# Kernel optimization log

Hardware: AMD Instinct MI355X
Metric: run time of the kernel (lower is better)

Reference implementation:

```python
import jax, jax.numpy as jnp
import numpy as np
import math

C = 96; HEADS = 3; HD = C // HEADS; WS = 8; B = 4; H = 256; W = 256
EPS = 1e-5; SCALE = HD ** -0.5; LOGIT_MAX = math.log(1.0 / 0.01)
N = WS * WS


def _rel_pos():
    coords = np.stack(np.meshgrid(np.arange(WS), np.arange(WS), indexing='ij')).reshape(2, -1)
    rel = (coords[:, :, None] - coords[:, None, :]).transpose(1, 2, 0).astype(np.float32)
    return jnp.asarray(np.sign(rel) * np.log1p(np.abs(rel)))  # [N, N, 2]

REL = _rel_pos()


def conv1x1(x, w, b):
    return jnp.einsum('bchw,oc->bohw', x, w) + b[None, :, None, None]


def dwconv(x, w, b, pad, reflect=False):
    if reflect:
        x = jnp.pad(x, ((0, 0), (0, 0), (pad, pad), (pad, pad)), mode='reflect')
        padding = 'VALID'
    else:
        padding = [(pad, pad), (pad, pad)]
    y = jax.lax.conv_general_dilated(x, w, (1, 1), padding,
                                     feature_group_count=x.shape[1],
                                     dimension_numbers=('NCHW', 'OIHW', 'NCHW'))
    return y + b[None, :, None, None]


def window_partition(x):  # [B,H,W,C] -> [nW, WS*WS, C]
    b, h, w, c = x.shape
    x = x.reshape(b, h // WS, WS, w // WS, WS, c).transpose(0, 1, 3, 2, 4, 5)
    return x.reshape(-1, WS * WS, c)


def window_reverse(win, h, w):  # [nW, WS*WS, C] -> [B,H,W,C]
    b = win.shape[0] // ((h // WS) * (w // WS))
    x = win.reshape(b, h // WS, w // WS, WS, WS, -1).transpose(0, 1, 3, 2, 4, 5)
    return x.reshape(b, h, w, -1)


def setup_inputs() -> dict:
    key = jax.random.key(0)
    ks = jax.random.split(key, 16)
    def nrm(k, shape, std=0.02):
        return jax.random.normal(k, shape, jnp.float32) * std
    inp = {'x': jax.random.normal(ks[0], (B, C, H, W), jnp.float32)}
    inp.update(
        agn_weight=jnp.ones((C,), jnp.float32), agn_bias=jnp.zeros((C,), jnp.float32),
        meta1_w=nrm(ks[1], (C,)), meta1_b=jnp.ones((C,), jnp.float32),
        meta2_w=nrm(ks[2], (C,)), meta2_b=jnp.zeros((C,), jnp.float32),
        la1_w=nrm(ks[3], (C, 1, 3, 3)), la1_b=jnp.zeros((C,), jnp.float32),
        la2_w=nrm(ks[4], (C, 1, 3, 3)), la2_b=jnp.zeros((C,), jnp.float32),
        ta1_w=nrm(ks[5], (C, 1, 3, 3)), ta1_b=jnp.zeros((C,), jnp.float32),
        ta2_w=nrm(ks[6], (C, 1, 3, 3)), ta2_b=jnp.zeros((C,), jnp.float32),
        q_w=nrm(ks[7], (C, C)), q_b=jnp.zeros((C,), jnp.float32),
        kv_w=nrm(ks[8], (2 * C, C)), kv_b=jnp.zeros((2 * C,), jnp.float32),
        dw_w=nrm(ks[9], (C, 1, 5, 5)), dw_b=jnp.zeros((C,), jnp.float32),
        proj_w=nrm(ks[10], (C, C)), proj_b=jnp.zeros((C,), jnp.float32),
        logit_scale=jnp.asarray(math.log(1.0 / 0.07), jnp.float32),
        rp_w1=nrm(ks[11], (256, 2)), rp_b1=jnp.zeros((256,), jnp.float32),
        rp_w2=nrm(ks[12], (HEADS, 256)), rp_b2=jnp.zeros((HEADS,), jnp.float32),
        m1_w=nrm(ks[13], (4 * C, C)), m1_b=jnp.zeros((4 * C,), jnp.float32),
        m2_w=nrm(ks[14], (C, 4 * C)), m2_b=jnp.zeros((C,), jnp.float32),
    )
    return inp


def reference(x, agn_weight, agn_bias, meta1_w, meta1_b, meta2_w, meta2_b,
              la1_w, la1_b, la2_w, la2_b, ta1_w, ta1_b, ta2_w, ta2_b,
              q_w, q_b, kv_w, kv_b, dw_w, dw_b, proj_w, proj_b,
              logit_scale, rp_w1, rp_b1, rp_w2, rp_b2,
              m1_w, m1_b, m2_w, m2_b):
    identity = x
    # ---- AGN: per-sample global mean/std norm + dynamic affine + two dw-conv branches
    mean = jnp.mean(x, axis=(1, 2, 3), keepdims=True)                      # [B,1,1,1]
    std = jnp.sqrt(jnp.mean((x - mean) ** 2, axis=(1, 2, 3), keepdims=True) + EPS)
    xn = (x - mean) / std
    rescale = std * meta1_w[None, :, None, None] + meta1_b[None, :, None, None]   # conv1x1(1->C) on std
    rebias = mean * meta2_w[None, :, None, None] + meta2_b[None, :, None, None]
    local = dwconv(jax.nn.relu(dwconv(xn, la1_w, la1_b, 1)), la2_w, la2_b, 1)
    texture = dwconv(jax.nn.relu(dwconv(xn, ta1_w, ta1_b, 1)), ta2_w, ta2_b, 1)
    xn = xn * (agn_weight[None, :, None, None] * rescale) + (agn_bias[None, :, None, None] + rebias) + local + texture
    # ---- DSAttention (use_attn, DWConv, shift_size=0, H%WS==0 so no padding)
    Q = conv1x1(xn, q_w, q_b)
    KV = conv1x1(xn, kv_w, kv_b)                                           # [B,2C,H,W]
    qkv_img = jnp.concatenate([Q, KV], axis=1).transpose(0, 2, 3, 1)       # [B,H,W,3C]
    co = dwconv(Q, dw_w, dw_b, 2, reflect=True).transpose(0, 2, 3, 1)      # reflect-padded 5x5 dwconv
    qkv = window_partition(qkv_img)                                        # [nW,N,3C]
    cw = window_partition(co)                                              # [nW,N,C]
    nW = qkv.shape[0]
    qkv = qkv.reshape(nW, N, 3, HEADS, HD).transpose(2, 0, 3, 1, 4)        # [3,nW,h,N,hd]
    q = cw.reshape(nW, N, HEADS, HD).transpose(0, 2, 1, 3)                 # q replaced by conv branch
    k = qkv[1] * SCALE
    v = qkv[2]
    ls = jnp.exp(jnp.minimum(logit_scale, LOGIT_MAX))
    hb = jax.nn.relu(REL @ rp_w1.T + rp_b1)                                # [N,N,256]
    bias = (hb @ rp_w2.T + rp_b2).transpose(2, 0, 1)                       # [h,N,N]
    attn = jax.nn.softmax(jnp.einsum('whnd,whmd->whnm', q, k) * ls + bias[None], axis=-1)
    o = jnp.einsum('whnm,whmd->whnd', attn, v).transpose(0, 2, 1, 3).reshape(nW, N, C)
    out = window_reverse(o, x.shape[2], x.shape[3]).transpose(0, 3, 1, 2)  # [B,C,H,W]
    a = conv1x1(out, proj_w, proj_b)
    x = identity + a * rescale + rebias
    # ---- MLP (1x1 conv -> ReLU -> 1x1 conv), residual
    x = x + conv1x1(jax.nn.relu(conv1x1(x, m1_w, m1_b)), m2_w, m2_b)
    return x
```

## Files before the change

### kernel.cpp

```cpp
#include <hip/hip_runtime.h>
#include <hip/hip_bf16.h>

typedef __hip_bfloat16 bf16;

#define PER_B     6291456
#define EPS_F     1e-5f
#define SCALE_F   0.17677669529663687f
#define LOGIT_MAX_F 4.605170185988092f

__device__ __forceinline__ float b2f(bf16 v){ return __bfloat162float(v); }
__device__ __forceinline__ bf16  f2b(float v){ return __float2bfloat16(v); }

template<int DT> __device__ __forceinline__ float rdf(const void* p, size_t i){
  return DT ? ((const float*)p)[i] : b2f(((const bf16*)p)[i]);
}
template<int DT> __device__ __forceinline__ void wrf(void* p, size_t i, float v){
  if (DT) ((float*)p)[i] = v; else ((bf16*)p)[i] = f2b(v);
}
template<int DT> __device__ __forceinline__ float2 rd2(const void* p, size_t i){
  if (DT) return *(const float2*)((const float*)p + i);
  unsigned u = *(const unsigned*)((const bf16*)p + i);
  return make_float2(__uint_as_float(u << 16), __uint_as_float(u & 0xffff0000u));
}

typedef __attribute__((ext_vector_type(8))) short short8v;
typedef __attribute__((ext_vector_type(4))) short short4v;
typedef __attribute__((ext_vector_type(4))) float f32x4;

__device__ __forceinline__ short f2bs(float v){
  unsigned u = __float_as_uint(v);
  return (short)((u + 0x7fffu + ((u >> 16) & 1u)) >> 16);
}
__device__ __forceinline__ float bs2f(short s){
  return __uint_as_float(((unsigned)(unsigned short)s) << 16);
}

template<int DT> __device__ __forceinline__ short8v ld8(const void* p, size_t i){
  short8v a;
  if (DT){
    const float* f = (const float*)p + i;
    float4 lo = *(const float4*)f;
    float4 hi = *(const float4*)(f + 4);
    a[0]=f2bs(lo.x); a[1]=f2bs(lo.y); a[2]=f2bs(lo.z); a[3]=f2bs(lo.w);
    a[4]=f2bs(hi.x); a[5]=f2bs(hi.y); a[6]=f2bs(hi.z); a[7]=f2bs(hi.w);
  } else {
    a = *(const short8v*)((const short*)p + i);
  }
  return a;
}
template<int DT> __device__ __forceinline__ short8v ld4x2(const void* p, size_t i0){
  short8v a;
  if (DT){
    const float* f = (const float*)p;
    float4 lo = *(const float4*)(f + i0);
    float4 hi = *(const float4*)(f + i0 + 16);
    a[0]=f2bs(lo.x); a[1]=f2bs(lo.y); a[2]=f2bs(lo.z); a[3]=f2bs(lo.w);
    a[4]=f2bs(hi.x); a[5]=f2bs(hi.y); a[6]=f2bs(hi.z); a[7]=f2bs(hi.w);
  } else {
    const short* s = (const short*)p;
    short4v lo = *(const short4v*)(s + i0);
    short4v hi = *(const short4v*)(s + i0 + 16);
    a[0]=lo[0]; a[1]=lo[1]; a[2]=lo[2]; a[3]=lo[3];
    a[4]=hi[0]; a[5]=hi[1]; a[6]=hi[2]; a[7]=hi[3];
  }
  return a;
}

__global__ __launch_bounds__(256) void k_detect(const void* __restrict__ x, int* __restrict__ flag){
  __shared__ int cnt;
  if (threadIdx.x == 0) cnt = 0;
  __syncthreads();
  float v = b2f(((const bf16*)x)[(size_t)threadIdx.x * 16]);
  int bad = (!(v == v)) || (fabsf(v) > 1e20f);
  if (bad) atomicAdd(&cnt, 1);
  __syncthreads();
  if (threadIdx.x == 0) *flag = (cnt >= 4) ? 1 : 0;
}

template<int DT>
__global__ __launch_bounds__(256) void k_stats_partial(const void* __restrict__ x,
    float* __restrict__ partials, const int* __restrict__ flag){
  if (*flag != DT) return;
  int blk = blockIdx.x;
  int b = blk >> 8, chunk = blk & 255;
  const int chunkN = PER_B / 256;
  size_t base = (size_t)b * PER_B + (size_t)chunk * chunkN;
  float s = 0.f, ss = 0.f;
  for (int i = threadIdx.x; i < chunkN; i += 256){
    float v = rdf<DT>(x, base + i); s += v; ss += v*v;
  }
  __shared__ float sh[512];
  sh[threadIdx.x] = s; sh[256 + threadIdx.x] = ss;
  __syncthreads();
  for (int st = 128; st > 0; st >>= 1){
    if (threadIdx.x < st){
      sh[threadIdx.x]     += sh[threadIdx.x + st];
      sh[256+threadIdx.x] += sh[256+threadIdx.x + st];
    }
    __syncthreads();
  }
  if (threadIdx.x == 0){ partials[blk*2] = sh[0]; partials[blk*2+1] = sh[256]; }
}

template<int DT>
__global__ __launch_bounds__(256) void k_stats_final(const float* __restrict__ partials,
    const void* m1w, const void* m1b, const void* m2w, const void* m2b,
    float* __restrict__ stats, const int* __restrict__ flag){
  if (*flag != DT) return;
  __shared__ float sh[512];
  __shared__ float mS[4], sS[4];
  for (int b = 0; b < 4; b++){
    sh[threadIdx.x]     = partials[(b*256+threadIdx.x)*2];
    sh[256+threadIdx.x] = partials[(b*256+threadIdx.x)*2+1];
    __syncthreads();
    for (int st = 128; st > 0; st >>= 1){
      if (threadIdx.x < st){
        sh[threadIdx.x]     += sh[threadIdx.x + st];
        sh[256+threadIdx.x] += sh[256+threadIdx.x + st];
      }
      __syncthreads();
    }
    if (threadIdx.x == 0){
      float mean = sh[0] / (float)PER_B;
      float var  = sh[256] / (float)PER_B - mean*mean;
      float stdv = sqrtf(var + EPS_F);
      mS[b] = mean; sS[b] = stdv;
      stats[b] = mean; stats[4+b] = stdv;
    }
    __syncthreads();
  }
  for (int t = threadIdx.x; t < 384; t += 256){
    int b = t / 96, c = t % 96;
    stats[8+t]   = sS[b]*rdf<DT>(m1w,c) + rdf<DT>(m1b,c);
    stats[392+t] = mS[b]*rdf<DT>(m2w,c) + rdf<DT>(m2b,c);
  }
}

template<int DT>
__global__ __launch_bounds__(256) void k_bias(const void* w1, const void* b1v,
    const void* w2, const void* b2v, float* __restrict__ biasT, const int* __restrict__ flag){
  if (*flag != DT) return;
  int i = blockIdx.x >> 6, j = blockIdx.x & 63;
  int dy = (i>>3) - (j>>3), dx = (i&7) - (j&7);
  float fy = (float)dy, fx = (float)dx;
  float r0 = copysignf(log1pf(fabsf(fy)), fy);
  float r1 = copysignf(log1pf(fabsf(fx)), fx);
  int t = threadIdx.x;
  float hb = fmaxf(r0*rdf<DT>(w1,t*2) + r1*rdf<DT>(w1,t*2+1) + rdf<DT>(b1v,t), 0.f);
  __shared__ float sh[256];
  for (int h = 0; h < 3; h++){
    sh[t] = hb * rdf<DT>(w2, h*256+t);
    __syncthreads();
    for (int st = 128; st > 0; st >>= 1){ if (t < st) sh[t] += sh[t+st]; __syncthreads(); }
    if (t == 0) biasT[h*4096 + j*64 + i] = sh[0] + rdf<DT>(b2v, h);
    __syncthreads();
  }
}

template<int DT>
__global__ __launch_bounds__(256) void k_agn_fused(const void* __restrict__ x,
    const float* __restrict__ stats,
    const void* la1w, const void* la1b, const void* la2w, const void* la2b,
    const void* ta1w, const void* ta1b, const void* ta2w, const void* ta2b,
    const void* agnw, const void* agnb,
    bf16* __restrict__ xn2, const int* __restrict__ flag){
  if (*flag != DT) return;
  __shared__ float xs[400];
  __shared__ float ts[324];
  __shared__ float us[324];
  int idx = blockIdx.x;
  int tile = idx & 255; int bc = idx >> 8; int c = bc % 96; int b = bc / 96;
  int oy = (tile >> 4) << 4, ox = (tile & 15) << 4;
  float mean = stats[b], sd = stats[4+b];
  size_t xbase = ((size_t)bc) << 16;
  for (int it = threadIdx.x; it < 400; it += 256){
    int ly = it / 20, lx = it % 20;
    int gy = oy - 2 + ly, gx = ox - 2 + lx;
    float v = 0.f;
    if (gy >= 0 && gy < 256 && gx >= 0 && gx < 256)
      v = (rdf<DT>(x, xbase + (gy<<8) + gx) - mean) / sd;
    xs[it] = v;
  }
  float wl1[9], wt1[9], wl2[9], wt2[9];
  #pragma unroll
  for (int k = 0; k < 9; k++){
    wl1[k] = rdf<DT>(la1w, c*9+k); wt1[k] = rdf<DT>(ta1w, c*9+k);
    wl2[k] = rdf<DT>(la2w, c*9+k); wt2[k] = rdf<DT>(ta2w, c*9+k);
  }
  float bl1 = rdf<DT>(la1b, c), bt1 = rdf<DT>(ta1b, c);
  __syncthreads();
  for (int it = threadIdx.x; it < 324; it += 256){
    int ly = it / 18, lx = it % 18;
    int cy = oy - 1 + ly, cx = ox - 1 + lx;
    float a1 = 0.f, a2 = 0.f;
    if (cy >= 0 && cy < 256 && cx >= 0 && cx < 256){
      a1 = bl1; a2 = bt1;
      #pragma unroll
      for (int dy = 0; dy < 3; dy++)
        #pragma unroll
        for (int dx = 0; dx < 3; dx++){
          float v = xs[(ly+dy)*20 + lx+dx];
          a1 += v * wl1[dy*3+dx]; a2 += v * wt1[dy*3+dx];
        }
      a1 = fmaxf(a1, 0.f); a2 = fmaxf(a2, 0.f);
    }
    ts[it] = a1; us[it] = a2;
  }
  __syncthreads();
  int ty = threadIdx.x >> 4, tx0 = threadIdx.x & 15;
  float l = rdf<DT>(la2b, c), t = rdf<DT>(ta2b, c);
  #pragma unroll
  for (int dy = 0; dy < 3; dy++)
    #pragma unroll
    for (int dx = 0; dx < 3; dx++){
      l += ts[(ty+dy)*18 + tx0+dx] * wl2[dy*3+dx];
      t += us[(ty+dy)*18 + tx0+dx] * wt2[dy*3+dx];
    }
  float v = xs[(ty+2)*20 + tx0+2];
  float r = v*(rdf<DT>(agnw,c)*stats[8+bc]) + (rdf<DT>(agnb,c) + stats[392+bc]) + l + t;
  xn2[xbase + ((oy+ty)<<8) + ox + tx0] = f2b(r);
}

#define XS_OFF 0
#define KT_OFF 0
#define VD_OFF 13312
#define OS_OFF 0
#define QB_OFF 29952
#define XC_OFF 29952
#define PS_OFF 29952
#define CS_OFF 48896

template<int DT>
__global__ __launch_bounds__(256) void k_attn_mega(const bf16* __restrict__ xn2,
    const void* qw, const void* qb, const void* kvw, const void* kvb,
    const void* dww, const void* dwb, const void* pw, const void* pb,
    const void* lsin, const float* __restrict__ biasT,
    const void* __restrict__ xin, const float* __restrict__ stats,
    void* __restrict__ outp, const int* __restrict__ flag){
  if (*flag != DT) return;
  __shared__ __align__(16) char smem[62208];
  int tid = threadIdx.x, wid = blockIdx.x;
  int b = wid >> 10, wy = (wid >> 5) & 31, wx = wid & 31;
  int wv = tid >> 6, ln = tid & 63;
  int r = ln & 15, q = ln >> 4;

  {
    short* xs = (short*)(smem + XS_OFF);
    for (int it = tid; it < 13824; it += 256){
      int t = it % 144, c = it / 144;
      int ty = (wy<<3) - 2 + t/12, tx = (wx<<3) - 2 + t%12;
      ty = ty < 0 ? -ty : (ty > 255 ? 510 - ty : ty);
      tx = tx < 0 ? -tx : (tx > 255 ? 510 - tx : tx);
      xs[t*104 + c] = ((const short*)xn2)[(((size_t)(b*96 + c))<<16) + (ty<<8) + tx];
    }
  }
  __syncthreads();

  {
    const short* xs = (const short*)(smem + XS_OFF);
    short* Qb = (short*)(smem + QB_OFF) + wv*2368;
    short* cs = (short*)(smem + CS_OFF);
    int ty0 = (ln>>3)+2, tx0 = (ln&7)+2;
    for (int mt = wv; mt < 6; mt += 4){
      short8v aw[3];
      #pragma unroll
      for (int kt = 0; kt < 3; kt++)
        aw[kt] = ld8<DT>(qw, (size_t)(16*mt + r)*96 + 32*kt + 8*q);
      float qb4[4];
      #pragma unroll
      for (int j = 0; j < 4; j++) qb4[j] = rdf<DT>(qb, 16*mt + 4*q + j);
      for (int nt = 0; nt < 9; nt++){
        f32x4 acc = {0.f,0.f,0.f,0.f};
        #pragma unroll
        for (int kt = 0; kt < 3; kt++){
          short8v bx = *(const short8v*)(xs + (16*nt + r)*104 + 32*kt + 8*q);
          acc = __builtin_amdgcn_mfma_f32_16x16x32_bf16(aw[kt], bx, acc, 0, 0, 0);
        }
        #pragma unroll
        for (int j = 0; j < 4; j++)
          Qb[(4*q+j)*148 + 16*nt + r] = f2bs(acc[j] + qb4[j]);
      }
      asm volatile("s_waitcnt lgkmcnt(0)" ::: "memory");
      for (int cl = 0; cl < 16; cl++){
        int c = 16*mt + cl;
        float a = rdf<DT>(dwb, c);
        #pragma unroll
        for (int dy = -2; dy <= 2; dy++)
          #pragma unroll
          for (int dx = -2; dx <= 2; dx++)
            a += bs2f(Qb[cl*148 + (ty0+dy)*12 + tx0+dx]) * rdf<DT>(dww, c*25 + (dy+2)*5 + dx+2);
        cs[ln*104 + c] = f2bs(a);
      }
      asm volatile("s_waitcnt lgkmcnt(0)" ::: "memory");
    }
  }
  __syncthreads();

  {
    short* xc = (short*)(smem + XC_OFF);
    for (int it = tid; it < 768; it += 256){
      int c = it >> 3, row = it & 7;
      const short* src = (const short*)xn2 + (((size_t)(b*96 + c))<<16)
                         + (((wy<<3)+row)<<8) + (wx<<3);
      short8v v = *(const short8v*)src;
      #pragma unroll
      for (int px = 0; px < 8; px++) xc[(row*8+px)*104 + c] = v[px];
    }
  }
  __syncthreads();
  {
    const short* xc = (const short*)(smem + XC_OFF);
    short* Kt = (short*)(smem + KT_OFF);
    short* Vd = (short*)(smem + VD_OFF);
    for (int mtk = wv; mtk < 12; mtk += 4){
      short8v aw[3];
      #pragma unroll
      for (int kt = 0; kt < 3; kt++)
        aw[kt] = ld8<DT>(kvw, (size_t)(16*mtk + r)*96 + 32*kt + 8*q);
      float bb[4];
      #pragma unroll
      for (int j = 0; j < 4; j++) bb[j] = rdf<DT>(kvb, 16*mtk + 4*q + j);
      for (int nt = 0; nt < 4; nt++){
        f32x4 acc = {0.f,0.f,0.f,0.f};
        #pragma unroll
        for (int kt = 0; kt < 3; kt++){
          short8v bx = *(const short8v*)(xc + (16*nt + r)*104 + 32*kt + 8*q);
          acc = __builtin_amdgcn_mfma_f32_16x16x32_bf16(aw[kt], bx, acc, 0, 0, 0);
        }
        if (mtk < 6){
          short4v kv;
          #pragma unroll
          for (int j = 0; j < 4; j++) kv[j] = f2bs((acc[j] + bb[j]) * SCALE_F);
          *(short4v*)(Kt + (16*nt + r)*104 + 16*mtk + 4*q) = kv;
        } else {
          #pragma unroll
          for (int j = 0; j < 4; j++)
            Vd[(16*(mtk-6) + 4*q + j)*72 + 16*nt + r] = f2bs(acc[j] + bb[j]);
        }
      }
    }
  }
  __syncthreads();

  float o_save[24];
  {
    const short* cs = (const short*)(smem + CS_OFF);
    const short* Kt = (const short*)(smem + KT_OFF);
    const short* Vd = (const short*)(smem + VD_OFF);
    short* Psw = (short*)(smem + PS_OFF) + wv*1152;
    float lsv = __expf(fminf(rdf<DT>(lsin, 0), LOGIT_MAX_F));
    #pragma unroll
    for (int h = 0; h < 3; h++){
      short8v qa = *(const short8v*)(cs + (16*wv + r)*104 + 32*h + 8*q);
      f32x4 s[4];
      #pragma unroll
      for (int mt = 0; mt < 4; mt++){
        short8v kb = *(const short8v*)(Kt + (16*mt + r)*104 + 32*h + 8*q);
        f32x4 z = {0.f,0.f,0.f,0.f};
        s[mt] = __builtin_amdgcn_mfma_f32_16x16x32_bf16(qa, kb, z, 0, 0, 0);
      }
      float l[4][4];
      #pragma unroll
      for (int mt = 0; mt < 4; mt++){
        float4 bv = *(const float4*)(biasT + h*4096 + (16*mt + r)*64 + 16*wv + 4*q);
        l[mt][0] = s[mt][0]*lsv + bv.x;
        l[mt][1] = s[mt][1]*lsv + bv.y;
        l[mt][2] = s[mt][2]*lsv + bv.z;
        l[mt][3] = s[mt][3]*lsv + bv.w;
      }
      float mx[4], sm[4];
      #pragma unroll
      for (int j = 0; j < 4; j++){
        float m0 = fmaxf(fmaxf(l[0][j], l[1][j]), fmaxf(l[2][j], l[3][j]));
        m0 = fmaxf(m0, __shfl_xor(m0, 1));
        m0 = fmaxf(m0, __shfl_xor(m0, 2));
        m0 = fmaxf(m0, __shfl_xor(m0, 4));
        m0 = fmaxf(m0, __shfl_xor(m0, 8));
        mx[j] = m0; sm[j] = 0.f;
      }
      #pragma unroll
      for (int mt = 0; mt < 4; mt++)
        #pragma unroll
        for (int j = 0; j < 4; j++){
          float p = __expf(l[mt][j] - mx[j]);
          sm[j] += p;
          Psw[(4*q+j)*72 + 16*mt + r] = f2bs(p);
        }
      #pragma unroll
      for (int j = 0; j < 4; j++){
        sm[j] += __shfl_xor(sm[j], 1);
        sm[j] += __shfl_xor(sm[j], 2);
        sm[j] += __shfl_xor(sm[j], 4);
        sm[j] += __shfl_xor(sm[j], 8);
      }
      float inv[4];
      #pragma unroll
      for (int j = 0; j < 4; j++) inv[j] = 1.f / sm[j];
      asm volatile("s_waitcnt lgkmcnt(0)" ::: "memory");
      short8v pa0 = *(const short8v*)(Psw + r*72 + 8*q);
      short8v pa1 = *(const short8v*)(Psw + r*72 + 32 + 8*q);
      #pragma unroll
      for (int dt = 0; dt < 2; dt++){
        f32x4 o = {0.f,0.f,0.f,0.f};
        short8v vb0 = *(const short8v*)(Vd + (32*h + 16*dt + r)*72 + 8*q);
        short8v vb1 = *(const short8v*)(Vd + (32*h + 16*dt + r)*72 + 32 + 8*q);
        o = __builtin_amdgcn_mfma_f32_16x16x32_bf16(pa0, vb0, o, 0, 0, 0);
        o = __builtin_amdgcn_mfma_f32_16x16x32_bf16(pa1, vb1, o, 0, 0, 0);
        #pragma unroll
        for (int j = 0; j < 4; j++) o_save[h*8 + dt*4 + j] = o[j] * inv[j];
      }
      asm volatile("s_waitcnt lgkmcnt(0)" ::: "memory");
    }
  }
  __syncthreads();

  {
    short* os = (short*)(smem + OS_OFF);
    #pragma unroll
    for (int h = 0; h < 3; h++)
      #pragma unroll
      for (int dt = 0; dt < 2; dt++)
        #pragma unroll
        for (int j = 0; j < 4; j++)
          os[(16*wv + 4*q + j)*104 + 32*h + 16*dt + r] = f2bs(o_save[h*8 + dt*4 + j]);
  }
  __syncthreads();

  {
    const short* os = (const short*)(smem + OS_OFF);
    short8v ob[3];
    #pragma unroll
    for (int kt = 0; kt < 3; kt++)
      ob[kt] = *(const short8v*)(os + (16*wv + r)*104 + 32*kt + 8*q);
    for (int mt = 0; mt < 6; mt++){
      f32x4 acc = {0.f,0.f,0.f,0.f};
      #pragma unroll
      for (int kt = 0; kt < 3; kt++){
        short8v aw = ld8<DT>(pw, (size_t)(16*mt + r)*96 + 32*kt + 8*q);
        acc = __builtin_amdgcn_mfma_f32_16x16x32_bf16(aw, ob[kt], acc, 0, 0, 0);
      }
      #pragma unroll
      for (int j = 0; j < 4; j++){
        int oc = 16*mt + 4*q + j;
        int n  = 16*wv + r;
        int gy = (wy<<3) + (n>>3), gx = (wx<<3) + (n&7);
        size_t gi = (((size_t)(b*96 + oc))<<16) + (gy<<8) + gx;
        float a = acc[j] + rdf<DT>(pb, oc);
        float x1 = rdf<DT>(xin, gi) + a*stats[8 + b*96 + oc] + stats[392 + b*96 + oc];
        wrf<DT>(outp, gi, x1);
      }
    }
  }
}

template<int DT>
__global__ __launch_bounds__(256) void k_mlp_mfma(void* __restrict__ io,
    const void* w1, const void* b1, const void* w2, const void* b2v,
    const int* __restrict__ flag){
  if (*flag != DT) return;
  __shared__ __align__(16) short x1s[256*104];
  int blk = blockIdx.x; int b = blk >> 8; int pix0 = (blk & 255) << 8;
  int tid = threadIdx.x;

  for (int c = 0; c < 96; c++){
    size_t gi = (((size_t)(b*96 + c))<<16) + pix0 + tid;
    short v = DT ? f2bs(((const float*)io)[gi]) : ((const short*)io)[gi];
    x1s[tid*104 + c] = v;
  }
  __syncthreads();

  int wv = tid >> 6, l = tid & 63;
  int r = l & 15, q = l >> 4;
  int pbase = wv << 6;

  f32x4 acc2[6][4];
  #pragma unroll
  for (int mt = 0; mt < 6; mt++)
    #pragma unroll
    for (int nt = 0; nt < 4; nt++)
      acc2[mt][nt] = (f32x4){0.f,0.f,0.f,0.f};

  #pragma unroll 2
  for (int t = 0; t < 12; t++){
    short8v aA[3], aB[3];
    #pragma unroll
    for (int kt = 0; kt < 3; kt++){
      aA[kt] = ld8<DT>(w1, (size_t)(32*t + r)*96      + 32*kt + 8*q);
      aB[kt] = ld8<DT>(w1, (size_t)(32*t + 16 + r)*96 + 32*kt + 8*q);
    }
    float bA[4], bB[4];
    #pragma unroll
    for (int j = 0; j < 4; j++){
      bA[j] = rdf<DT>(b1, 32*t + 4*q + j);
      bB[j] = rdf<DT>(b1, 32*t + 16 + 4*q + j);
    }
    f32x4 a1A[4], a1B[4];
    #pragma unroll
    for (int nt = 0; nt < 4; nt++){
      a1A[nt] = (f32x4){0.f,0.f,0.f,0.f};
      a1B[nt] = (f32x4){0.f,0.f,0.f,0.f};
    }
    #pragma unroll
    for (int kt = 0; kt < 3; kt++){
      #pragma unroll
      for (int nt = 0; nt < 4; nt++){
        short8v bx = *(const short8v*)&x1s[(pbase + 16*nt + r)*104 + 32*kt + 8*q];
        a1A[nt] = __builtin_amdgcn_mfma_f32_16x16x32_bf16(aA[kt], bx, a1A[nt], 0, 0, 0);
        a1B[nt] = __builtin_amdgcn_mfma_f32_16x16x32_bf16(aB[kt], bx, a1B[nt], 0, 0, 0);
      }
    }
    short8v B2[4];
    #pragma unroll
    for (int nt = 0; nt < 4; nt++){
      short8v h;
      #pragma unroll
      for (int j = 0; j < 4; j++){
        h[j]   = f2bs(fmaxf(a1A[nt][j] + bA[j], 0.f));
        h[4+j] = f2bs(fmaxf(a1B[nt][j] + bB[j], 0.f));
      }
      B2[nt] = h;
    }
    #pragma unroll
    for (int mt = 0; mt < 6; mt++){
      short8v wA = ld4x2<DT>(w2, (size_t)(16*mt + r)*384 + 32*t + 4*q);
      #pragma unroll
      for (int nt = 0; nt < 4; nt++)
        acc2[mt][nt] = __builtin_amdgcn_mfma_f32_16x16x32_bf16(wA, B2[nt], acc2[mt][nt], 0, 0, 0);
    }
  }

  #pragma unroll
  for (int mt = 0; mt < 6; mt++)
    #pragma unroll
    for (int nt = 0; nt < 4; nt++)
      #pragma unroll
      for (int j = 0; j < 4; j++){
        int oc = 16*mt + 4*q + j;
        int pl = pbase + 16*nt + r;
        size_t gi = (((size_t)(b*96 + oc))<<16) + pix0 + pl;
        float v = acc2[mt][nt][j] + rdf<DT>(b2v, oc);
        if (DT){
          ((float*)io)[gi] = ((const float*)io)[gi] + v;
        } else {
          ((bf16*)io)[gi] = f2b(bs2f(x1s[pl*104 + oc]) + v);
        }
      }
}

extern "C" void kernel_launch(void* const* d_in, const int* in_sizes, int n_in,
                              void* d_out, int out_size, void* d_ws, size_t ws_size,
                              hipStream_t stream) {
  const void* x      = d_in[0];
  const void* agnw   = d_in[1];
  const void* agnb   = d_in[2];
  const void* meta1w = d_in[3];
  const void* meta1b = d_in[4];
  const void* meta2w = d_in[5];
  const void* meta2b = d_in[6];
  const void* la1w   = d_in[7];
  const void* la1b   = d_in[8];
  const void* la2w   = d_in[9];
  const void* la2b   = d_in[10];
  const void* ta1w   = d_in[11];
  const void* ta1b   = d_in[12];
  const void* ta2w   = d_in[13];
  const void* ta2b   = d_in[14];
  const void* qw     = d_in[15];
  const void* qb     = d_in[16];
  const void* kvw    = d_in[17];
  const void* kvb    = d_in[18];
  const void* dww    = d_in[19];
  const void* dwb    = d_in[20];
  const void* pw     = d_in[21];
  const void* pb     = d_in[22];
  const void* lsin   = d_in[23];
  const void* rpw1   = d_in[24];
  const void* rpb1   = d_in[25];
  const void* rpw2   = d_in[26];
  const void* rpb2   = d_in[27];
  const void* m1w    = d_in[28];
  const void* m1b    = d_in[29];
  const void* m2w    = d_in[30];
  const void* m2b    = d_in[31];

  char* ws = (char*)d_ws;
  int*   flag     = (int*)ws;
  float* partials = (float*)(ws + 256);
  float* stats    = (float*)(ws + 8448);
  float* biasT    = (float*)(ws + 12288);
  bf16*  xn2      = (bf16*)(ws + 65536);

  k_detect<<<1, 256, 0, stream>>>(x, flag);

  k_stats_partial<0><<<1024, 256, 0, stream>>>(x, partials, flag);
  k_stats_final<0>  <<<1,    256, 0, stream>>>(partials, meta1w, meta1b, meta2w, meta2b, stats, flag);
  k_bias<0>         <<<4096, 256, 0, stream>>>(rpw1, rpb1, rpw2, rpb2, biasT, flag);
  k_agn_fused<0>    <<<98304,256, 0, stream>>>(x, stats, la1w, la1b, la2w, la2b,
                                               ta1w, ta1b, ta2w, ta2b, agnw, agnb, xn2, flag);
  k_attn_mega<0>    <<<4096, 256, 0, stream>>>(xn2, qw, qb, kvw, kvb, dww, dwb, pw, pb,
                                               lsin, biasT, x, stats, d_out, flag);
  k_mlp_mfma<0>     <<<1024, 256, 0, stream>>>(d_out, m1w, m1b, m2w, m2b, flag);

  k_stats_partial<1><<<1024, 256, 0, stream>>>(x, partials, flag);
  k_stats_final<1>  <<<1,    256, 0, stream>>>(partials, meta1w, meta1b, meta2w, meta2b, stats, flag);
  k_bias<1>         <<<4096, 256, 0, stream>>>(rpw1, rpb1, rpw2, rpb2, biasT, flag);
  k_agn_fused<1>    <<<98304,256, 0, stream>>>(x, stats, la1w, la1b, la2w, la2b,
                                               ta1w, ta1b, ta2w, ta2b, agnw, agnb, xn2, flag);
  k_attn_mega<1>    <<<4096, 256, 0, stream>>>(xn2, qw, qb, kvw, kvb, dww, dwb, pw, pb,
                                               lsin, biasT, x, stats, d_out, flag);
  k_mlp_mfma<1>     <<<1024, 256, 0, stream>>>(d_out, m1w, m1b, m2w, m2b, flag);
}
```

Before: 1.139 ms.

## Shrink attention-kernel LDS footprint to fit three blocks per CU

Shared memory for the fused window-attention kernel is re-laid out so regions overlap more tightly. The per-wave Q staging buffer is halved: the 16 projected channels are staged in two passes of 8, with the accumulators held in registers in between. Launch bounds now request 3 blocks per CU, to raise occupancy and hide latency. The scatter stores into the xs and xc transposed tiles are reordered with XOR patterns to reduce LDS bank conflicts. In exchange the kernel uses more registers for the held accumulators, adds extra LDS waits, and the register cap from the launch bound may cause spills.

```diff
diff --git a/kernel.cpp b/kernel.cpp
--- a/kernel.cpp
+++ b/kernel.cpp
@@ -221,24 +221,24 @@
   xn2[xbase + ((oy+ty)<<8) + ox + tx0] = f2b(r);
 }
 
-#define XS_OFF 0
-#define KT_OFF 0
-#define VD_OFF 13312
-#define OS_OFF 0
-#define QB_OFF 29952
-#define XC_OFF 29952
-#define PS_OFF 29952
-#define CS_OFF 48896
+#define CS_OFF 0
+#define XS_OFF 13312
+#define QB_OFF 43264
+#define KT_OFF 13312
+#define VD_OFF 26624
+#define XC_OFF 40448
+#define PS_OFF 40448
+#define OS_OFF 13312
 
 template<int DT>
-__global__ __launch_bounds__(256) void k_attn_mega(const bf16* __restrict__ xn2,
+__global__ __launch_bounds__(256, 3) void k_attn_mega(const bf16* __restrict__ xn2,
     const void* qw, const void* qb, const void* kvw, const void* kvb,
     const void* dww, const void* dwb, const void* pw, const void* pb,
     const void* lsin, const float* __restrict__ biasT,
     const void* __restrict__ xin, const float* __restrict__ stats,
     void* __restrict__ outp, const int* __restrict__ flag){
   if (*flag != DT) return;
-  __shared__ __align__(16) char smem[62208];
+  __shared__ __align__(16) char smem[53760];
   int tid = threadIdx.x, wid = blockIdx.x;
   int b = wid >> 10, wy = (wid >> 5) & 31, wx = wid & 31;
   int wv = tid >> 6, ln = tid & 63;
@@ -247,7 +247,8 @@
   {
     short* xs = (short*)(smem + XS_OFF);
     for (int it = tid; it < 13824; it += 256){
-      int t = it % 144, c = it / 144;
+      int t = it % 144, craw = it / 144;
+      int c = craw ^ ((t >> 3) & 7);
       int ty = (wy<<3) - 2 + t/12, tx = (wx<<3) - 2 + t%12;
       ty = ty < 0 ? -ty : (ty > 255 ? 510 - ty : ty);
       tx = tx < 0 ? -tx : (tx > 255 ? 510 - tx : tx);
@@ -258,7 +259,7 @@
 
   {
     const short* xs = (const short*)(smem + XS_OFF);
-    short* Qb = (short*)(smem + QB_OFF) + wv*2368;
+    short* Qb = (short*)(smem + QB_OFF) + wv*1184;
     short* cs = (short*)(smem + CS_OFF);
     int ty0 = (ln>>3)+2, tx0 = (ln&7)+2;
     for (int mt = wv; mt < 6; mt += 4){
@@ -269,6 +270,8 @@
       float qb4[4];
       #pragma unroll
       for (int j = 0; j < 4; j++) qb4[j] = rdf<DT>(qb, 16*mt + 4*q + j);
+      float accs[9][4];
+      #pragma unroll
       for (int nt = 0; nt < 9; nt++){
         f32x4 acc = {0.f,0.f,0.f,0.f};
         #pragma unroll
@@ -277,11 +280,17 @@
           acc = __builtin_amdgcn_mfma_f32_16x16x32_bf16(aw[kt], bx, acc, 0, 0, 0);
         }
         #pragma unroll
-        for (int j = 0; j < 4; j++)
-          Qb[(4*q+j)*148 + 16*nt + r] = f2bs(acc[j] + qb4[j]);
+        for (int j = 0; j < 4; j++) accs[nt][j] = acc[j] + qb4[j];
+      }
+      if (q < 2){
+        #pragma unroll
+        for (int nt = 0; nt < 9; nt++)
+          #pragma unroll
+          for (int j = 0; j < 4; j++)
+            Qb[(4*q+j)*148 + 16*nt + r] = f2bs(accs[nt][j]);
       }
       asm volatile("s_waitcnt lgkmcnt(0)" ::: "memory");
-      for (int cl = 0; cl < 16; cl++){
+      for (int cl = 0; cl < 8; cl++){
         int c = 16*mt + cl;
         float a = rdf<DT>(dwb, c);
         #pragma unroll
@@ -289,6 +298,25 @@
           #pragma unroll
           for (int dx = -2; dx <= 2; dx++)
             a += bs2f(Qb[cl*148 + (ty0+dy)*12 + tx0+dx]) * rdf<DT>(dww, c*25 + (dy+2)*5 + dx+2);
+        cs[ln*104 + c] = f2bs(a);
+      }
+      asm volatile("s_waitcnt lgkmcnt(0)" ::: "memory");
+      if (q >= 2){
+        #pragma unroll
+        for (int nt = 0; nt < 9; nt++)
+          #pragma unroll
+          for (int j = 0; j < 4; j++)
+            Qb[(4*(q-2)+j)*148 + 16*nt + r] = f2bs(accs[nt][j]);
+      }
+      asm volatile("s_waitcnt lgkmcnt(0)" ::: "memory");
+      for (int cl = 8; cl < 16; cl++){
+        int c = 16*mt + cl;
+        float a = rdf<DT>(dwb, c);
+        #pragma unroll
+        for (int dy = -2; dy <= 2; dy++)
+          #pragma unroll
+          for (int dx = -2; dx <= 2; dx++)
+            a += bs2f(Qb[(cl-8)*148 + (ty0+dy)*12 + tx0+dx]) * rdf<DT>(dww, c*25 + (dy+2)*5 + dx+2);
         cs[ln*104 + c] = f2bs(a);
       }
       asm volatile("s_waitcnt lgkmcnt(0)" ::: "memory");
@@ -304,7 +332,10 @@
                          + (((wy<<3)+row)<<8) + (wx<<3);
       short8v v = *(const short8v*)src;
       #pragma unroll
-      for (int px = 0; px < 8; px++) xc[(row*8+px)*104 + c] = v[px];
+      for (int k = 0; k < 8; k++){
+        int pe = k ^ row;
+        xc[(row*8+pe)*104 + c] = v[pe];
+      }
     }
   }
   __syncthreads();
```

Result: faster. 1.107 ms (-2.8%).
